# Performance work log

Measured on AMD Instinct MI355X. Metric: run time of the kernel, lower is better.

Reference implementation:

```python
import jax, jax.numpy as jnp
import numpy as np

N_EMBD = 1024
N_HEAD = 16
HEAD_DIM = N_EMBD // N_HEAD


def setup_inputs() -> dict:
    key = jax.random.key(0)
    k1, k2, k3, k4, k5 = jax.random.split(key, 5)
    x = jax.random.normal(k1, (4, 2048, N_EMBD), dtype=jnp.float32)
    s_in = 1.0 / np.sqrt(N_EMBD)
    W_attn = jax.random.normal(k2, (N_EMBD, 3 * N_EMBD), dtype=jnp.float32) * s_in
    b_attn = jax.random.normal(k3, (3 * N_EMBD,), dtype=jnp.float32) * 0.01
    W_proj = jax.random.normal(k4, (N_EMBD, N_EMBD), dtype=jnp.float32) * s_in
    b_proj = jax.random.normal(k5, (N_EMBD,), dtype=jnp.float32) * 0.01
    return {"x": x, "W_attn": W_attn, "b_attn": b_attn, "W_proj": W_proj, "b_proj": b_proj}


def reference(x, W_attn, b_attn, W_proj, b_proj):
    B, T, C = x.shape
    qkv = jnp.einsum('btc,cd->btd', x, W_attn) + b_attn  # [B,T,3C]
    q, k, v = jnp.split(qkv, 3, axis=2)
    # [B,T,C] -> [B,H,T,Dh]
    def heads(t):
        return t.reshape(B, T, N_HEAD, HEAD_DIM).transpose(0, 2, 1, 3)
    q, k, v = heads(q), heads(k), heads(v)
    scale = HEAD_DIM ** -0.5
    att = jnp.einsum('bhqd,bhkd->bhqk', q, k) * scale  # [B,H,T,T]
    causal = jnp.tril(jnp.ones((T, T), dtype=bool))
    att = jnp.where(causal[None, None], att, -jnp.inf)
    att = jax.nn.softmax(att, axis=-1)
    y = jnp.einsum('bhqk,bhkd->bhqd', att, v)  # [B,H,T,Dh]
    y = y.transpose(0, 2, 1, 3).reshape(B, T, C)
    y = jnp.einsum('btc,cd->btd', y, W_proj) + b_proj
    return y
```

## Files before the change

### kernel.cpp

```cpp
#include <hip/hip_runtime.h>

typedef unsigned short u16;
typedef unsigned int u32;
typedef __bf16 bf16x8 __attribute__((ext_vector_type(8)));
typedef u16 u16x8 __attribute__((ext_vector_type(8)));
typedef u16 u16x4 __attribute__((ext_vector_type(4)));
typedef float f32x4 __attribute__((ext_vector_type(4)));
typedef float f32x16 __attribute__((ext_vector_type(16)));

#define BHTD 8388608
#define QSCALE 0.18033688f

__device__ __forceinline__ u16 f2bf(float f) {
  union { float f; u32 u; } x; x.f = f;
  u32 r = (x.u + 0x7FFFu + ((x.u >> 16) & 1u)) >> 16;
  return (u16)r;
}

__device__ __forceinline__ u32 cvt_pk_bf16(float lo, float hi) {
  u32 r;
  asm("v_cvt_pk_bf16_f32 %0, %1, %2" : "=v"(r) : "v"(lo), "v"(hi));
  return r;
}

__device__ __forceinline__ void permlane32_swap(u32& x, u32& y) {
  asm("v_permlane32_swap_b32 %0, %1" : "+v"(x), "+v"(y));
}

__device__ __forceinline__ void async_copy16(const u16* gsrc, u16* ldst) {
  __builtin_amdgcn_global_load_lds(
      (const __attribute__((address_space(1))) void*)gsrc,
      (__attribute__((address_space(3))) void*)ldst, 16, 0, 0);
}

__global__ __launch_bounds__(256) void conv_x_kernel(const float4* __restrict__ in,
                                                     u16x4* __restrict__ out, int n4) {
  int i = blockIdx.x * 256 + threadIdx.x;
  int stride = gridDim.x * 256;
  for (; i < n4; i += stride) {
    float4 v = in[i];
    u16x4 o = { f2bf(v.x), f2bf(v.y), f2bf(v.z), f2bf(v.w) };
    out[i] = o;
  }
}

__global__ __launch_bounds__(256) void transpose_bf16(const float* __restrict__ W,
                                                      u16* __restrict__ Wt, int K, int N) {
  __shared__ float t[64][65];
  int c0 = blockIdx.x * 64;
  int r0 = blockIdx.y * 64;
  int c = threadIdx.x & 63;
  int r4 = threadIdx.x >> 6;
#pragma unroll
  for (int j = 0; j < 16; ++j) {
    int r = j * 4 + r4;
    t[r][c] = W[(size_t)(r0 + r) * N + (c0 + c)];
  }
  __syncthreads();
#pragma unroll
  for (int j = 0; j < 16; ++j) {
    int n = j * 4 + r4;
    Wt[(size_t)(c0 + n) * K + (r0 + c)] = f2bf(t[c][n]);
  }
}

template <int MODE>
__global__ __launch_bounds__(256) void gemm_bf16(const u16* __restrict__ A,
                                                 const u16* __restrict__ Bt,
                                                 const float* __restrict__ bias,
                                                 float* __restrict__ outp,
                                                 u16* __restrict__ qkv, int grid_n) {
  __shared__ __attribute__((aligned(16))) u16 A_lds[128 * 64];
  __shared__ __attribute__((aligned(16))) u16 B_lds[128 * 64];
  const int tid = threadIdx.x;
  const int lane = tid & 63, wave = tid >> 6;
  const int wr = wave >> 1, wc = wave & 1;
  const int bn = blockIdx.x % grid_n, bm = blockIdx.x / grid_n;
  const int m0 = bm * 128, n0 = bn * 128;
  const int g = lane >> 4, c16 = lane & 15;
  const int lrow = lane >> 3, lslot = lane & 7;

  f32x4 acc[4][4] = {};

  for (int kt = 0; kt < 16; ++kt) {
#pragma unroll
    for (int i = 0; i < 4; ++i) {
      int mloc = (wave * 4 + i) * 8 + lrow;
      int col = kt * 64 + ((lslot ^ (mloc & 7)) << 3);
      async_copy16(&A[(size_t)(m0 + mloc) * 1024 + col], &A_lds[(wave * 4 + i) * 512]);
      async_copy16(&Bt[(size_t)(n0 + mloc) * 1024 + col], &B_lds[(wave * 4 + i) * 512]);
    }
    __syncthreads();
#pragma unroll
    for (int kk = 0; kk < 2; ++kk) {
      bf16x8 af[4], bfr[4];
#pragma unroll
      for (int mb = 0; mb < 4; ++mb) {
        int row = wr * 64 + mb * 16 + c16;
        int slot = (kk * 4 + g) ^ (row & 7);
        af[mb] = *(const bf16x8*)&A_lds[row * 64 + slot * 8];
        int rowb = wc * 64 + mb * 16 + c16;
        int slotb = (kk * 4 + g) ^ (rowb & 7);
        bfr[mb] = *(const bf16x8*)&B_lds[rowb * 64 + slotb * 8];
      }
#pragma unroll
      for (int mb = 0; mb < 4; ++mb)
#pragma unroll
        for (int nb = 0; nb < 4; ++nb)
          acc[mb][nb] = __builtin_amdgcn_mfma_f32_16x16x32_bf16(af[mb], bfr[nb], acc[mb][nb], 0, 0, 0);
    }
    __syncthreads();
  }

  float bv[4];
#pragma unroll
  for (int nb = 0; nb < 4; ++nb) bv[nb] = bias[n0 + wc * 64 + nb * 16 + c16];

#pragma unroll
  for (int mb = 0; mb < 4; ++mb) {
    int row0 = m0 + wr * 64 + mb * 16 + g * 4;
#pragma unroll
    for (int nb = 0; nb < 4; ++nb) {
      int col = n0 + wc * 64 + nb * 16 + c16;
      float bvn = bv[nb];
      if (MODE == 0) {
        int sel = col >> 10, ci = col & 1023;
        int hh = ci >> 6, d = ci & 63;
        int bb = row0 >> 11, t0 = row0 & 2047;
        float qs = (sel == 0) ? QSCALE : 1.0f;
        if (sel == 2) {
          u16x4 pk;
#pragma unroll
          for (int r = 0; r < 4; ++r) pk[r] = f2bf(acc[mb][nb][r] + bvn);
          *(u16x4*)&qkv[(size_t)2 * BHTD + (((size_t)(bb * 16 + hh) * 64 + d) << 11) + t0] = pk;
        } else {
#pragma unroll
          for (int r = 0; r < 4; ++r) {
            qkv[(size_t)sel * BHTD + (((size_t)(bb * 16 + hh) * 2048 + t0 + r) << 6) + d] =
                f2bf((acc[mb][nb][r] + bvn) * qs);
          }
        }
      } else {
#pragma unroll
        for (int r = 0; r < 4; ++r)
          outp[((size_t)(row0 + r) << 10) + col] = acc[mb][nb][r] + bvn;
      }
    }
  }
}

__global__ __launch_bounds__(256, 4) void attn_fwd(const u16* __restrict__ Q,
                                                   const u16* __restrict__ K,
                                                   const u16* __restrict__ VT,
                                                   u16* __restrict__ Y) {
  __shared__ __attribute__((aligned(16))) u16 Kl[2][64 * 64];
  __shared__ __attribute__((aligned(16))) u16 Vl[2][64 * 64];
  const float NEG_INF = -__builtin_inff();

  int bid = blockIdx.x;
  int j = bid >> 6, hd = bid & 63;
  int qt = (j < 4) ? (15 - j) : (j < 8) ? (j - 4) : (j < 12) ? j : (19 - j);
  size_t hb = (size_t)hd * (2048 * 64);
  const u16* Qh = Q + hb;
  const u16* Kh = K + hb;
  const u16* Vh = VT + hb;
  int tid = threadIdx.x, lane = tid & 63, w = tid >> 6;
  int c32 = lane & 31, h = lane >> 5;
  int qw0 = qt * 128 + w * 32;
  int qrow = qw0 + c32;
  int qend = qw0 + 32;
  int nt = 2 * qt + 2;

  int ch0 = tid, ch1 = tid + 256;
  int sr0 = ch0 >> 3, sw0 = ((ch0 & 7) ^ (sr0 & 7)) << 3;
  int sr1 = ch1 >> 3, sw1 = ((ch1 & 7) ^ (sr1 & 7)) << 3;

  bf16x8 qf[4];
#pragma unroll
  for (int dk = 0; dk < 4; ++dk)
    qf[dk] = *(const bf16x8*)&Qh[(size_t)qrow * 64 + dk * 16 + 8 * h];

  float m = NEG_INF, l = 0.f;
  f32x16 o0 = {}, o1 = {};

  async_copy16(&Kh[(size_t)sr0 * 64 + sw0], &Kl[0][ch0 << 3]);
  async_copy16(&Kh[(size_t)sr1 * 64 + sw1], &Kl[0][ch1 << 3]);
  async_copy16(&Vh[(size_t)sr0 * 2048 + sw0], &Vl[0][ch0 << 3]);
  async_copy16(&Vh[(size_t)sr1 * 2048 + sw1], &Vl[0][ch1 << 3]);

  const int xs = c32 & 7;

  for (int it = 0; it < nt; ++it) {
    int kv0 = it << 6;
    int cb = it & 1;
    __syncthreads();

    if (it + 1 < nt) {
      int kv1 = kv0 + 64;
      async_copy16(&Kh[(size_t)(kv1 + sr0) * 64 + sw0], &Kl[cb ^ 1][ch0 << 3]);
      async_copy16(&Kh[(size_t)(kv1 + sr1) * 64 + sw1], &Kl[cb ^ 1][ch1 << 3]);
      async_copy16(&Vh[(size_t)sr0 * 2048 + kv1 + sw0], &Vl[cb ^ 1][ch0 << 3]);
      async_copy16(&Vh[(size_t)sr1 * 2048 + kv1 + sw1], &Vl[cb ^ 1][ch1 << 3]);
    }
    if (kv0 >= qend) continue;

    bf16x8 kf[2][4];
#pragma unroll
    for (int kb = 0; kb < 2; ++kb)
#pragma unroll
      for (int dk = 0; dk < 4; ++dk)
        kf[kb][dk] =
            *(const bf16x8*)&Kl[cb][(kb * 32 + c32) * 64 + (((2 * dk + h) ^ xs) << 3)];
    f32x16 s0 = {}, s1 = {};
    __builtin_amdgcn_s_setprio(1);
#pragma unroll
    for (int dk = 0; dk < 4; ++dk) {
      s0 = __builtin_amdgcn_mfma_f32_32x32x16_bf16(kf[0][dk], qf[dk], s0, 0, 0, 0);
      s1 = __builtin_amdgcn_mfma_f32_32x32x16_bf16(kf[1][dk], qf[dk], s1, 0, 0, 0);
    }
    __builtin_amdgcn_s_setprio(0);

    if (kv0 + 64 >= qend) {
      int kvb = kv0 + 4 * h;
#pragma unroll
      for (int reg = 0; reg < 16; ++reg) {
        int kvl = kvb + 8 * (reg >> 2) + (reg & 3);
        if (kvl > qrow) s0[reg] = NEG_INF;
        if (kvl + 32 > qrow) s1[reg] = NEG_INF;
      }
    }

    float a0 = fmaxf(s0[0], s1[0]), a1 = fmaxf(s0[1], s1[1]);
    float a2 = fmaxf(s0[2], s1[2]), a3 = fmaxf(s0[3], s1[3]);
#pragma unroll
    for (int i = 4; i < 16; i += 4) {
      a0 = fmaxf(a0, fmaxf(s0[i], s1[i]));
      a1 = fmaxf(a1, fmaxf(s0[i + 1], s1[i + 1]));
      a2 = fmaxf(a2, fmaxf(s0[i + 2], s1[i + 2]));
      a3 = fmaxf(a3, fmaxf(s0[i + 3], s1[i + 3]));
    }
    float rm = fmaxf(fmaxf(a0, a1), fmaxf(a2, a3));
    rm = fmaxf(rm, __shfl_xor(rm, 32));
    if (__any(rm - m > 8.f)) {
      float mn = fmaxf(m, rm);
      float alpha = __builtin_exp2f(m - mn);
      l *= alpha;
      o0 *= alpha;
      o1 *= alpha;
      m = mn;
    }
#pragma unroll
    for (int i = 0; i < 16; ++i) s0[i] = __builtin_exp2f(s0[i] - m);
#pragma unroll
    for (int i = 0; i < 16; ++i) s1[i] = __builtin_exp2f(s1[i] - m);
    float b0 = s0[0] + s1[0], b1 = s0[1] + s1[1], b2 = s0[2] + s1[2], b3 = s0[3] + s1[3];
#pragma unroll
    for (int i = 4; i < 16; i += 4) {
      b0 += s0[i] + s1[i];
      b1 += s0[i + 1] + s1[i + 1];
      b2 += s0[i + 2] + s1[i + 2];
      b3 += s0[i + 3] + s1[i + 3];
    }
    float rs = (b0 + b1) + (b2 + b3);
    rs += __shfl_xor(rs, 32);
    l += rs;

    u32 pw0[8], pw1[8];
#pragma unroll
    for (int mm = 0; mm < 8; ++mm) {
      pw0[mm] = cvt_pk_bf16(s0[2 * mm], s0[2 * mm + 1]);
      pw1[mm] = cvt_pk_bf16(s1[2 * mm], s1[2 * mm + 1]);
    }
    permlane32_swap(pw0[0], pw0[2]); permlane32_swap(pw0[1], pw0[3]);
    permlane32_swap(pw0[4], pw0[6]); permlane32_swap(pw0[5], pw0[7]);
    permlane32_swap(pw1[0], pw1[2]); permlane32_swap(pw1[1], pw1[3]);
    permlane32_swap(pw1[4], pw1[6]); permlane32_swap(pw1[5], pw1[7]);

    __builtin_amdgcn_s_setprio(1);
#pragma unroll
    for (int c = 0; c < 4; ++c) {
      const u32* pp = (c >> 1) ? pw1 : pw0;
      const int a = 4 * (c & 1);
      union { u32 u[4]; bf16x8 v; } pf;
      pf.u[0] = pp[a + 0];
      pf.u[1] = pp[a + 1];
      pf.u[2] = pp[a + 2];
      pf.u[3] = pp[a + 3];
      bf16x8 vf0 = *(const bf16x8*)&Vl[cb][c32 * 64 + (((2 * c + h) ^ xs) << 3)];
      bf16x8 vf1 = *(const bf16x8*)&Vl[cb][(32 + c32) * 64 + (((2 * c + h) ^ xs) << 3)];
      o0 = __builtin_amdgcn_mfma_f32_32x32x16_bf16(vf0, pf.v, o0, 0, 0, 0);
      o1 = __builtin_amdgcn_mfma_f32_32x32x16_bf16(vf1, pf.v, o1, 0, 0, 0);
    }
    __builtin_amdgcn_s_setprio(0);
  }

  float inv = 1.0f / l;
  size_t yb = (size_t)(hd >> 4) * (2048 * 1024) + (size_t)(hd & 15) * 64 + (size_t)qrow * 1024;
#pragma unroll
  for (int db = 0; db < 2; ++db)
#pragma unroll
    for (int rq = 0; rq < 4; ++rq) {
      u16x4 pk;
#pragma unroll
      for (int jj = 0; jj < 4; ++jj)
        pk[jj] = f2bf((db ? o1[rq * 4 + jj] : o0[rq * 4 + jj]) * inv);
      *(u16x4*)&Y[yb + db * 32 + 8 * rq + 4 * h] = pk;
    }
}

extern "C" void kernel_launch(void* const* d_in, const int* in_sizes, int n_in,
                              void* d_out, int out_size, void* d_ws, size_t ws_size,
                              hipStream_t stream) {
  (void)in_sizes; (void)n_in; (void)out_size; (void)ws_size;
  const float* x      = (const float*)d_in[0];
  const float* W_attn = (const float*)d_in[1];
  const float* b_attn = (const float*)d_in[2];
  const float* W_proj = (const float*)d_in[3];
  const float* b_proj = (const float*)d_in[4];
  float* out = (float*)d_out;

  char* ws = (char*)d_ws;
  u16* Xb  = (u16*)(ws);
  u16* Wt  = (u16*)(ws + 16777216);
  u16* Wpt = (u16*)(ws + 16777216 + 6291456);
  u16* QKV = (u16*)(ws + 16777216 + 6291456 + 2097152);
  u16* Yb  = Xb;

  conv_x_kernel<<<2048, 256, 0, stream>>>((const float4*)x, (u16x4*)Xb, 2097152);
  transpose_bf16<<<dim3(48, 16), 256, 0, stream>>>(W_attn, Wt, 1024, 3072);
  transpose_bf16<<<dim3(16, 16), 256, 0, stream>>>(W_proj, Wpt, 1024, 1024);
  gemm_bf16<0><<<1536, 256, 0, stream>>>(Xb, Wt, b_attn, nullptr, QKV, 24);
  attn_fwd<<<1024, 256, 0, stream>>>(QKV, QKV + BHTD, QKV + 2 * BHTD, Yb);
  gemm_bf16<1><<<512, 256, 0, stream>>>(Yb, Wpt, b_proj, out, nullptr, 8);
}
```

Before: 186.0 us.

## Restructure attention into paired 64-row query tiles with direct V loads

Each attention block now has two waves and handles two 64-row query tiles (t and 31-t), so every block does the same amount of causal work. Before, four waves shared one 128-row tile under a hand-written tile order. V tiles are no longer staged in LDS. They are read straight from global memory into registers and prefetched one chunk ahead, which halves LDS use. The mask value changes from -inf to a large negative number. In exchange there are fewer waves per block, K tiles are reused by fewer waves, and V reads go to global memory with a stride of 2048 elements.

```diff
diff --git a/kernel.cpp b/kernel.cpp
--- a/kernel.cpp
+++ b/kernel.cpp
@@ -149,163 +149,177 @@
   }
 }
 
-__global__ __launch_bounds__(256, 4) void attn_fwd(const u16* __restrict__ Q,
+__global__ __launch_bounds__(128, 4) void attn_fwd(const u16* __restrict__ Q,
                                                    const u16* __restrict__ K,
                                                    const u16* __restrict__ VT,
                                                    u16* __restrict__ Y) {
   __shared__ __attribute__((aligned(16))) u16 Kl[2][64 * 64];
-  __shared__ __attribute__((aligned(16))) u16 Vl[2][64 * 64];
-  const float NEG_INF = -__builtin_inff();
+  const float NEG_BIG = -1e30f;
 
   int bid = blockIdx.x;
-  int j = bid >> 6, hd = bid & 63;
-  int qt = (j < 4) ? (15 - j) : (j < 8) ? (j - 4) : (j < 12) ? j : (19 - j);
+  int pj = bid >> 6, hd = bid & 63;
   size_t hb = (size_t)hd * (2048 * 64);
   const u16* Qh = Q + hb;
   const u16* Kh = K + hb;
   const u16* Vh = VT + hb;
   int tid = threadIdx.x, lane = tid & 63, w = tid >> 6;
   int c32 = lane & 31, h = lane >> 5;
-  int qw0 = qt * 128 + w * 32;
-  int qrow = qw0 + c32;
-  int qend = qw0 + 32;
-  int nt = 2 * qt + 2;
-
-  int ch0 = tid, ch1 = tid + 256;
-  int sr0 = ch0 >> 3, sw0 = ((ch0 & 7) ^ (sr0 & 7)) << 3;
-  int sr1 = ch1 >> 3, sw1 = ((ch1 & 7) ^ (sr1 & 7)) << 3;
-
-  bf16x8 qf[4];
-#pragma unroll
-  for (int dk = 0; dk < 4; ++dk)
-    qf[dk] = *(const bf16x8*)&Qh[(size_t)qrow * 64 + dk * 16 + 8 * h];
-
-  float m = NEG_INF, l = 0.f;
-  f32x16 o0 = {}, o1 = {};
-
-  async_copy16(&Kh[(size_t)sr0 * 64 + sw0], &Kl[0][ch0 << 3]);
-  async_copy16(&Kh[(size_t)sr1 * 64 + sw1], &Kl[0][ch1 << 3]);
-  async_copy16(&Vh[(size_t)sr0 * 2048 + sw0], &Vl[0][ch0 << 3]);
-  async_copy16(&Vh[(size_t)sr1 * 2048 + sw1], &Vl[0][ch1 << 3]);
-
   const int xs = c32 & 7;
 
-  for (int it = 0; it < nt; ++it) {
-    int kv0 = it << 6;
-    int cb = it & 1;
-    __syncthreads();
-
-    if (it + 1 < nt) {
-      int kv1 = kv0 + 64;
-      async_copy16(&Kh[(size_t)(kv1 + sr0) * 64 + sw0], &Kl[cb ^ 1][ch0 << 3]);
-      async_copy16(&Kh[(size_t)(kv1 + sr1) * 64 + sw1], &Kl[cb ^ 1][ch1 << 3]);
-      async_copy16(&Vh[(size_t)sr0 * 2048 + kv1 + sw0], &Vl[cb ^ 1][ch0 << 3]);
-      async_copy16(&Vh[(size_t)sr1 * 2048 + kv1 + sw1], &Vl[cb ^ 1][ch1 << 3]);
+  int ch[4], sr[4], sw[4];
+#pragma unroll
+  for (int i = 0; i < 4; ++i) {
+    ch[i] = tid + 128 * i;
+    sr[i] = ch[i] >> 3;
+    sw[i] = ((ch[i] & 7) ^ (sr[i] & 7)) << 3;
+  }
+
+  for (int pass = 0; pass < 2; ++pass) {
+    const int t64 = pass ? pj : 31 - pj;
+    const int nt = t64 + 1;
+    const int qw0 = t64 * 64 + w * 32;
+    const int qrow = qw0 + c32;
+
+    bf16x8 qf[4];
+#pragma unroll
+    for (int dk = 0; dk < 4; ++dk)
+      qf[dk] = *(const bf16x8*)&Qh[(size_t)qrow * 64 + dk * 16 + 8 * h];
+
+#pragma unroll
+    for (int i = 0; i < 4; ++i)
+      async_copy16(&Kh[(size_t)sr[i] * 64 + sw[i]], &Kl[0][ch[i] << 3]);
+
+    float m = NEG_BIG, l = 0.f;
+    f32x16 o0 = {}, o1 = {};
+
+    for (int it = 0; it < nt; ++it) {
+      int kv0 = it << 6;
+      int cb = it & 1;
+      __syncthreads();
+
+      if (it + 1 < nt) {
+        int kv1 = kv0 + 64;
+#pragma unroll
+        for (int i = 0; i < 4; ++i)
+          async_copy16(&Kh[(size_t)(kv1 + sr[i]) * 64 + sw[i]], &Kl[cb ^ 1][ch[i] << 3]);
+      }
+
+      bf16x8 kf[2][4];
+#pragma unroll
+      for (int kb = 0; kb < 2; ++kb)
+#pragma unroll
+        for (int dk = 0; dk < 4; ++dk)
+          kf[kb][dk] =
+              *(const bf16x8*)&Kl[cb][(kb * 32 + c32) * 64 + (((2 * dk + h) ^ xs) << 3)];
+      f32x16 s0 = {}, s1 = {};
+      __builtin_amdgcn_s_setprio(1);
+#pragma unroll
+      for (int dk = 0; dk < 4; ++dk) {
+        s0 = __builtin_amdgcn_mfma_f32_32x32x16_bf16(kf[0][dk], qf[dk], s0, 0, 0, 0);
+        s1 = __builtin_amdgcn_mfma_f32_32x32x16_bf16(kf[1][dk], qf[dk], s1, 0, 0, 0);
+      }
+      __builtin_amdgcn_s_setprio(0);
+
+      if (it + 1 == nt) {
+        int kvb = kv0 + 4 * h;
+#pragma unroll
+        for (int reg = 0; reg < 16; ++reg) {
+          int kvl = kvb + 8 * (reg >> 2) + (reg & 3);
+          if (kvl > qrow) s0[reg] = NEG_BIG;
+          if (kvl + 32 > qrow) s1[reg] = NEG_BIG;
+        }
+      }
+
+      float a0 = fmaxf(s0[0], s1[0]), a1 = fmaxf(s0[1], s1[1]);
+      float a2 = fmaxf(s0[2], s1[2]), a3 = fmaxf(s0[3], s1[3]);
+#pragma unroll
+      for (int i = 4; i < 16; i += 4) {
+        a0 = fmaxf(a0, fmaxf(s0[i], s1[i]));
+        a1 = fmaxf(a1, fmaxf(s0[i + 1], s1[i + 1]));
+        a2 = fmaxf(a2, fmaxf(s0[i + 2], s1[i + 2]));
+        a3 = fmaxf(a3, fmaxf(s0[i + 3], s1[i + 3]));
+      }
+      float rm = fmaxf(fmaxf(a0, a1), fmaxf(a2, a3));
+      rm = fmaxf(rm, __shfl_xor(rm, 32));
+      if (__any(rm - m > 8.f)) {
+        float mn = fmaxf(m, rm);
+        float alpha = __builtin_exp2f(m - mn);
+        l *= alpha;
+        o0 *= alpha;
+        o1 *= alpha;
+        m = mn;
+      }
+#pragma unroll
+      for (int i = 0; i < 16; ++i) s0[i] = __builtin_exp2f(s0[i] - m);
+#pragma unroll
+      for (int i = 0; i < 16; ++i) s1[i] = __builtin_exp2f(s1[i] - m);
+      float b0 = s0[0] + s1[0], b1 = s0[1] + s1[1];
+      float b2 = s0[2] + s1[2], b3 = s0[3] + s1[3];
+#pragma unroll
+      for (int i = 4; i < 16; i += 4) {
+        b0 += s0[i] + s1[i];
+        b1 += s0[i + 1] + s1[i + 1];
+        b2 += s0[i + 2] + s1[i + 2];
+        b3 += s0[i + 3] + s1[i + 3];
+      }
+      float rs = (b0 + b1) + (b2 + b3);
+      rs += __shfl_xor(rs, 32);
+      l += rs;
+
+      u32 pw0[8], pw1[8];
+#pragma unroll
+      for (int mm = 0; mm < 8; ++mm) {
+        pw0[mm] = cvt_pk_bf16(s0[2 * mm], s0[2 * mm + 1]);
+        pw1[mm] = cvt_pk_bf16(s1[2 * mm], s1[2 * mm + 1]);
+      }
+      permlane32_swap(pw0[0], pw0[2]); permlane32_swap(pw0[1], pw0[3]);
+      permlane32_swap(pw0[4], pw0[6]); permlane32_swap(pw0[5], pw0[7]);
+      permlane32_swap(pw1[0], pw1[2]); permlane32_swap(pw1[1], pw1[3]);
+      permlane32_swap(pw1[4], pw1[6]); permlane32_swap(pw1[5], pw1[7]);
+
+      bf16x8 va[2], vb[2];
+#pragma unroll
+      for (int c = 0; c < 2; ++c) {
+        va[c] = *(const bf16x8*)&Vh[(size_t)c32 * 2048 + kv0 + c * 16 + 8 * h];
+        vb[c] = *(const bf16x8*)&Vh[(size_t)(32 + c32) * 2048 + kv0 + c * 16 + 8 * h];
+      }
+      __builtin_amdgcn_s_setprio(1);
+#pragma unroll
+      for (int c = 0; c < 4; ++c) {
+        const u32* pp = (c >> 1) ? pw1 : pw0;
+        const int a = 4 * (c & 1);
+        union { u32 u[4]; bf16x8 v; } pf;
+        pf.u[0] = pp[a + 0];
+        pf.u[1] = pp[a + 1];
+        pf.u[2] = pp[a + 2];
+        pf.u[3] = pp[a + 3];
+        bf16x8 vfa = va[c & 1], vfb = vb[c & 1];
+        if (c < 2) {
+          va[c] = *(const bf16x8*)&Vh[(size_t)c32 * 2048 + kv0 + (c + 2) * 16 + 8 * h];
+          vb[c] = *(const bf16x8*)&Vh[(size_t)(32 + c32) * 2048 + kv0 + (c + 2) * 16 + 8 * h];
+        }
+        o0 = __builtin_amdgcn_mfma_f32_32x32x16_bf16(vfa, pf.v, o0, 0, 0, 0);
+        o1 = __builtin_amdgcn_mfma_f32_32x32x16_bf16(vfb, pf.v, o1, 0, 0, 0);
+      }
+      __builtin_amdgcn_s_setprio(0);
     }
-    if (kv0 >= qend) continue;
-
-    bf16x8 kf[2][4];
-#pragma unroll
-    for (int kb = 0; kb < 2; ++kb)
-#pragma unroll
-      for (int dk = 0; dk < 4; ++dk)
-        kf[kb][dk] =
-            *(const bf16x8*)&Kl[cb][(kb * 32 + c32) * 64 + (((2 * dk + h) ^ xs) << 3)];
-    f32x16 s0 = {}, s1 = {};
-    __builtin_amdgcn_s_setprio(1);
-#pragma unroll
-    for (int dk = 0; dk < 4; ++dk) {
-      s0 = __builtin_amdgcn_mfma_f32_32x32x16_bf16(kf[0][dk], qf[dk], s0, 0, 0, 0);
-      s1 = __builtin_amdgcn_mfma_f32_32x32x16_bf16(kf[1][dk], qf[dk], s1, 0, 0, 0);
-    }
-    __builtin_amdgcn_s_setprio(0);
-
-    if (kv0 + 64 >= qend) {
-      int kvb = kv0 + 4 * h;
-#pragma unroll
-      for (int reg = 0; reg < 16; ++reg) {
-        int kvl = kvb + 8 * (reg >> 2) + (reg & 3);
-        if (kvl > qrow) s0[reg] = NEG_INF;
-        if (kvl + 32 > qrow) s1[reg] = NEG_INF;
-      }
-    }
-
-    float a0 = fmaxf(s0[0], s1[0]), a1 = fmaxf(s0[1], s1[1]);
-    float a2 = fmaxf(s0[2], s1[2]), a3 = fmaxf(s0[3], s1[3]);
-#pragma unroll
-    for (int i = 4; i < 16; i += 4) {
-      a0 = fmaxf(a0, fmaxf(s0[i], s1[i]));
-      a1 = fmaxf(a1, fmaxf(s0[i + 1], s1[i + 1]));
-      a2 = fmaxf(a2, fmaxf(s0[i + 2], s1[i + 2]));
-      a3 = fmaxf(a3, fmaxf(s0[i + 3], s1[i + 3]));
-    }
-    float rm = fmaxf(fmaxf(a0, a1), fmaxf(a2, a3));
-    rm = fmaxf(rm, __shfl_xor(rm, 32));
-    if (__any(rm - m > 8.f)) {
-      float mn = fmaxf(m, rm);
-      float alpha = __builtin_exp2f(m - mn);
-      l *= alpha;
-      o0 *= alpha;
-      o1 *= alpha;
-      m = mn;
-    }
-#pragma unroll
-    for (int i = 0; i < 16; ++i) s0[i] = __builtin_exp2f(s0[i] - m);
-#pragma unroll
-    for (int i = 0; i < 16; ++i) s1[i] = __builtin_exp2f(s1[i] - m);
-    float b0 = s0[0] + s1[0], b1 = s0[1] + s1[1], b2 = s0[2] + s1[2], b3 = s0[3] + s1[3];
-#pragma unroll
-    for (int i = 4; i < 16; i += 4) {
-      b0 += s0[i] + s1[i];
-      b1 += s0[i + 1] + s1[i + 1];
-      b2 += s0[i + 2] + s1[i + 2];
-      b3 += s0[i + 3] + s1[i + 3];
-    }
-    float rs = (b0 + b1) + (b2 + b3);
-    rs += __shfl_xor(rs, 32);
-    l += rs;
-
-    u32 pw0[8], pw1[8];
-#pragma unroll
-    for (int mm = 0; mm < 8; ++mm) {
-      pw0[mm] = cvt_pk_bf16(s0[2 * mm], s0[2 * mm + 1]);
-      pw1[mm] = cvt_pk_bf16(s1[2 * mm], s1[2 * mm + 1]);
-    }
-    permlane32_swap(pw0[0], pw0[2]); permlane32_swap(pw0[1], pw0[3]);
-    permlane32_swap(pw0[4], pw0[6]); permlane32_swap(pw0[5], pw0[7]);
-    permlane32_swap(pw1[0], pw1[2]); permlane32_swap(pw1[1], pw1[3]);
-    permlane32_swap(pw1[4], pw1[6]); permlane32_swap(pw1[5], pw1[7]);
-
-    __builtin_amdgcn_s_setprio(1);
-#pragma unroll
-    for (int c = 0; c < 4; ++c) {
-      const u32* pp = (c >> 1) ? pw1 : pw0;
-      const int a = 4 * (c & 1);
-      union { u32 u[4]; bf16x8 v; } pf;
-      pf.u[0] = pp[a + 0];
-      pf.u[1] = pp[a + 1];
-      pf.u[2] = pp[a + 2];
-      pf.u[3] = pp[a + 3];
-      bf16x8 vf0 = *(const bf16x8*)&Vl[cb][c32 * 64 + (((2 * c + h) ^ xs) << 3)];
-      bf16x8 vf1 = *(const bf16x8*)&Vl[cb][(32 + c32) * 64 + (((2 * c + h) ^ xs) << 3)];
-      o0 = __builtin_amdgcn_mfma_f32_32x32x16_bf16(vf0, pf.v, o0, 0, 0, 0);
-      o1 = __builtin_amdgcn_mfma_f32_32x32x16_bf16(vf1, pf.v, o1, 0, 0, 0);
-    }
-    __builtin_amdgcn_s_setprio(0);
-  }
-
-  float inv = 1.0f / l;
-  size_t yb = (size_t)(hd >> 4) * (2048 * 1024) + (size_t)(hd & 15) * 64 + (size_t)qrow * 1024;
-#pragma unroll
-  for (int db = 0; db < 2; ++db)
-#pragma unroll
-    for (int rq = 0; rq < 4; ++rq) {
-      u16x4 pk;
-#pragma unroll
-      for (int jj = 0; jj < 4; ++jj)
-        pk[jj] = f2bf((db ? o1[rq * 4 + jj] : o0[rq * 4 + jj]) * inv);
-      *(u16x4*)&Y[yb + db * 32 + 8 * rq + 4 * h] = pk;
-    }
+
+    float inv = 1.0f / l;
+    size_t yb =
+        (size_t)(hd >> 4) * (2048 * 1024) + (size_t)(hd & 15) * 64 + (size_t)qrow * 1024;
+#pragma unroll
+    for (int db = 0; db < 2; ++db)
+#pragma unroll
+      for (int rq = 0; rq < 4; ++rq) {
+        u16x4 pk;
+#pragma unroll
+        for (int jj = 0; jj < 4; ++jj)
+          pk[jj] = f2bf((db ? o1[rq * 4 + jj] : o0[rq * 4 + jj]) * inv);
+        *(u16x4*)&Y[yb + db * 32 + 8 * rq + 4 * h] = pk;
+      }
+
+    if (pass == 0) __syncthreads();
+  }
 }
 
 extern "C" void kernel_launch(void* const* d_in, const int* in_sizes, int n_in,
@@ -330,6 +344,6 @@
   transpose_bf16<<<dim3(48, 16), 256, 0, stream>>>(W_attn, Wt, 1024, 3072);
   transpose_bf16<<<dim3(16, 16), 256, 0, stream>>>(W_proj, Wpt, 1024, 1024);
   gemm_bf16<0><<<1536, 256, 0, stream>>>(Xb, Wt, b_attn, nullptr, QKV, 24);
-  attn_fwd<<<1024, 256, 0, stream>>>(QKV, QKV + BHTD, QKV + 2 * BHTD, Yb);
+  attn_fwd<<<1024, 128, 0, stream>>>(QKV, QKV + BHTD, QKV + 2 * BHTD, Yb);
   gemm_bf16<1><<<512, 256, 0, stream>>>(Yb, Wpt, b_proj, out, nullptr, 8);
 }
```

New measurement: 246.6 us. +32.6%, slower.
